# Performance work log

Measured on AMD Instinct MI355X. Metric: run time of the kernel, lower is better.

Reference implementation:

```python
import jax, jax.numpy as jnp
import numpy as np

SL, BS, HS = 2048, 2, 1024
FFN, E, TOP_K = 4096, 8, 2


def setup_inputs() -> dict:
    key = jax.random.key(0)
    k1, k2, k3, k4, k5 = jax.random.split(key, 5)
    x = jax.random.normal(k1, (SL, BS, HS), dtype=jnp.float32)
    expert_weights = jax.random.uniform(k2, (SL * BS, TOP_K), dtype=jnp.float32)
    expert_indices = jax.random.randint(k3, (SL * BS, TOP_K), 0, E, dtype=jnp.int32)
    w1 = jax.random.normal(k4, (E, HS, FFN), dtype=jnp.float32) * 0.02
    w2 = jax.random.normal(k5, (E, FFN, HS), dtype=jnp.float32) * 0.02
    return {"x": x, "expert_weights": expert_weights,
            "expert_indices": expert_indices, "w1": w1, "w2": w2}


def reference(x, expert_weights, expert_indices, w1, w2):
    # Dropless MoE: y[t] = sum_k expert_weights[t,k] * MLP_{expert_indices[t,k]}(x[t])
    # Equivalent to megablocks sort/gather/grouped-GEMM/scatter pipeline, expressed
    # as a fixed loop over the (small) expert axis with masked weighted combine.
    sl, bs, hs = x.shape
    xf = x.reshape(-1, hs)                       # [T, hs]
    ew = expert_weights.reshape(xf.shape[0], -1)  # [T, k]
    ei = expert_indices.reshape(xf.shape[0], -1)  # [T, k]
    out = jnp.zeros_like(xf)
    for e in range(w1.shape[0]):
        h = jnp.dot(jax.nn.gelu(jnp.dot(xf, w1[e])), w2[e])   # [T, hs]
        coef = jnp.sum(jnp.where(ei == e, ew, 0.0), axis=-1)  # [T]
        out = out + coef[:, None] * h
    return out.reshape(sl, bs, hs)
```

## Files before the change

kernel.cpp:

```cpp
#include <hip/hip_runtime.h>
#include <stdint.h>

#define SLEN 2048
#define BSZ  2
#define HSZ  1024
#define FFND 4096
#define NEXP 8
#define TOPK 2
#define NTOK (SLEN*BSZ)
#define NSLOT (NTOK*TOPK)

#define BM 128
#define BN 128
#define BK 32
#define SPLITK 2
#define KS (FFND / SPLITK)

using short8 = __attribute__((ext_vector_type(8))) short;
using f32x4  = __attribute__((ext_vector_type(4))) float;

typedef __attribute__((address_space(1))) const unsigned int gu32;
typedef __attribute__((address_space(3))) unsigned int lu32;

__device__ inline void async_copy16(const void* g, void* l){
  __builtin_amdgcn_global_load_lds((gu32*)g, (lu32*)l, 16, 0, 0);
}

__device__ inline unsigned short f2bf(float f){
  unsigned u = __builtin_bit_cast(unsigned, f);
  u += 0x7FFFu + ((u >> 16) & 1u);
  return (unsigned short)(u >> 16);
}

__device__ inline float gelu_tanh(float x){
  float u = 0.7978845608028654f * (x + 0.044715f * x * x * x);
  return 0.5f * x * (1.0f + tanhf(u));
}


__global__ void k_count(const int* __restrict__ ei, int* __restrict__ counts){
  int i = blockIdx.x * blockDim.x + threadIdx.x;
  if (i < NSLOT) atomicAdd(&counts[ei[i]], 1);
}

__global__ void k_scan(const int* __restrict__ counts, int* __restrict__ offsets,
                       int* __restrict__ fill){
  if (threadIdx.x == 0 && blockIdx.x == 0){
    int acc = 0;
    for (int e = 0; e < NEXP; e++){ offsets[e] = acc; fill[e] = acc; acc += counts[e]; }
  }
}

__global__ void k_assign(const int* __restrict__ ei, const float* __restrict__ ew,
                         int* __restrict__ fill, int* __restrict__ rowT,
                         float* __restrict__ rowC){
  int i = blockIdx.x * blockDim.x + threadIdx.x;
  if (i < NSLOT){
    int e = ei[i];
    int slot = atomicAdd(&fill[e], 1);
    rowT[slot] = i >> 1;
    rowC[slot] = ew[i];
  }
}

__global__ void k_gather(const float* __restrict__ x, const int* __restrict__ rowT,
                         unsigned short* __restrict__ Xg){
  int slot = blockIdx.x;
  int t = rowT[slot];
  int c = threadIdx.x * 4;
  float4 v = *(const float4*)(x + (size_t)t * HSZ + c);
  ushort4 o;
  o.x = f2bf(v.x); o.y = f2bf(v.y); o.z = f2bf(v.z); o.w = f2bf(v.w);
  *(ushort4*)(Xg + (size_t)slot * HSZ + c) = o;
}

__global__ __launch_bounds__(256) void k_transpose2(const float* __restrict__ w1,
                                                    const float* __restrict__ w2,
                                                    unsigned short* __restrict__ Wt1,
                                                    unsigned short* __restrict__ Wt2){
  __shared__ unsigned short tile[64][65];
  const int tid = threadIdx.x;
  int z = blockIdx.y;
  const float* src; unsigned short* dst; int R, C, r0, c0;
  if (z < NEXP){
    src = w1 + (size_t)z * HSZ * FFND; dst = Wt1 + (size_t)z * HSZ * FFND;
    R = HSZ; C = FFND;
    c0 = (blockIdx.x & 63) * 64; r0 = (blockIdx.x >> 6) * 64;
  } else {
    z -= NEXP;
    src = w2 + (size_t)z * FFND * HSZ; dst = Wt2 + (size_t)z * FFND * HSZ;
    R = FFND; C = HSZ;
    c0 = (blockIdx.x & 15) * 64; r0 = (blockIdx.x >> 4) * 64;
  }
  #pragma unroll
  for (int p = 0; p < 4; p++){
    int r  = p * 16 + (tid >> 4);
    int cc = (tid & 15) * 4;
    float4 v = *(const float4*)(src + (size_t)(r0 + r) * C + c0 + cc);
    tile[r][cc]   = f2bf(v.x);
    tile[r][cc+1] = f2bf(v.y);
    tile[r][cc+2] = f2bf(v.z);
    tile[r][cc+3] = f2bf(v.w);
  }
  __syncthreads();
  #pragma unroll
  for (int p = 0; p < 4; p++){
    int c  = p * 16 + (tid >> 4);
    int rr = (tid & 15) * 4;
    ushort4 o;
    o.x = tile[rr][c]; o.y = tile[rr+1][c]; o.z = tile[rr+2][c]; o.w = tile[rr+3][c];
    *(ushort4*)(dst + (size_t)(c0 + c) * R + r0 + rr) = o;
  }
}

__device__ inline void gemm_core(const unsigned short* __restrict__ Ag, int lda, int rows,
                                 const unsigned short* __restrict__ Bg, int ldb, int K,
                                 unsigned short* As, unsigned short* Bs,
                                 f32x4 acc[4][4])
{
  const int tid  = threadIdx.x;
  const int lane = tid & 63;
  const int wid  = tid >> 6;
  const int wm   = (wid & 1) * 64;
  const int wn   = (wid >> 1) * 64;
  const int q    = lane >> 4;
  const int l16  = lane & 15;

  for (int k0 = 0; k0 < K; k0 += BK){
    #pragma unroll
    for (int p = 0; p < 2; p++){
      int c  = (wid * 2 + p) * 64 + lane;
      int r  = c >> 2;
      int kp = (c & 3) * 8;
      int ra = min(r, rows - 1);
      async_copy16(Ag + (size_t)ra * lda + k0 + kp, As + (wid * 2 + p) * 512);
      async_copy16(Bg + (size_t)r  * ldb + k0 + kp, Bs + (wid * 2 + p) * 512);
    }
    __syncthreads();

    short8 af[4], bfr[4];
    #pragma unroll
    for (int i = 0; i < 4; i++)
      af[i] = *(const short8*)(As + (wm + i * 16 + l16) * BK + q * 8);
    #pragma unroll
    for (int j = 0; j < 4; j++)
      bfr[j] = *(const short8*)(Bs + (wn + j * 16 + l16) * BK + q * 8);

    #pragma unroll
    for (int i = 0; i < 4; i++)
      #pragma unroll
      for (int j = 0; j < 4; j++)
        acc[i][j] = __builtin_amdgcn_mfma_f32_16x16x32_bf16(af[i], bfr[j], acc[i][j], 0, 0, 0);
    __syncthreads();
  }
}

__global__ __launch_bounds__(256) void k_gemm1(const unsigned short* __restrict__ Xg,
                                               const unsigned short* __restrict__ Wt1,
                                               unsigned short* __restrict__ H,
                                               const int* __restrict__ counts,
                                               const int* __restrict__ offsets)
{
  __shared__ unsigned short smem[BM * BK + BN * BK];
  unsigned short* As = smem;
  unsigned short* Bs = smem + BM * BK;
  const int e    = blockIdx.z;
  const int cnt  = counts[e];
  const int mblk = blockIdx.y;
  if (mblk * BM >= cnt) return;
  const int n0   = blockIdx.x * BN;
  const int row0 = offsets[e] + mblk * BM;
  const int rows = min(BM, cnt - mblk * BM);

  f32x4 acc[4][4] = {};
  gemm_core(Xg + (size_t)row0 * HSZ, HSZ, rows,
            Wt1 + (size_t)e * HSZ * FFND + (size_t)n0 * HSZ, HSZ, HSZ, As, Bs, acc);

  const int lane = threadIdx.x & 63, wid = threadIdx.x >> 6;
  const int wm = (wid & 1) * 64, wn = (wid >> 1) * 64;
  const int q = lane >> 4, l16 = lane & 15;

  unsigned short* scr = smem + wid * (16 * 68);
  #pragma unroll
  for (int i = 0; i < 4; i++){
    #pragma unroll
    for (int j = 0; j < 4; j++)
      #pragma unroll
      for (int r = 0; r < 4; r++)
        scr[(q * 4 + r) * 68 + j * 16 + l16] = f2bf(gelu_tanh(acc[i][j][r]));
    #pragma unroll
    for (int p = 0; p < 2; p++){
      int rr = p * 8 + (lane >> 3);
      int cc = (lane & 7) * 8;
      short8 v = *(const short8*)(scr + rr * 68 + cc);
      int grow = wm + i * 16 + rr;
      if (grow < rows)
        *(short8*)(H + (size_t)(row0 + grow) * FFND + n0 + wn + cc) = v;
    }
  }
}

__global__ __launch_bounds__(256) void k_gemm2(const unsigned short* __restrict__ H,
                                               const unsigned short* __restrict__ Wt2,
                                               float* __restrict__ out,
                                               const int* __restrict__ counts,
                                               const int* __restrict__ offsets,
                                               const int* __restrict__ rowT,
                                               const float* __restrict__ rowC)
{
  __shared__ unsigned short As[BM * BK];
  __shared__ unsigned short Bs[BN * BK];
  const int e    = blockIdx.z >> 1;
  const int s    = blockIdx.z & 1;
  const int cnt  = counts[e];
  const int mblk = blockIdx.y;
  if (mblk * BM >= cnt) return;
  const int n0   = blockIdx.x * BN;
  const int row0 = offsets[e] + mblk * BM;
  const int rows = min(BM, cnt - mblk * BM);

  f32x4 acc[4][4] = {};
  gemm_core(H + (size_t)row0 * FFND + (size_t)s * KS, FFND, rows,
            Wt2 + (size_t)e * FFND * HSZ + (size_t)n0 * FFND + (size_t)s * KS,
            FFND, KS, As, Bs, acc);

  const int lane = threadIdx.x & 63, wid = threadIdx.x >> 6;
  const int wm = (wid & 1) * 64, wn = (wid >> 1) * 64;
  const int q = lane >> 4, l16 = lane & 15;
  #pragma unroll
  for (int i = 0; i < 4; i++)
    #pragma unroll
    for (int j = 0; j < 4; j++)
      #pragma unroll
      for (int r = 0; r < 4; r++){
        int row = wm + i * 16 + q * 4 + r;
        if (row < rows){
          int g = row0 + row;
          int col = wn + j * 16 + l16;
          atomicAdd(out + (size_t)rowT[g] * HSZ + n0 + col, rowC[g] * acc[i][j][r]);
        }
      }
}

static inline size_t align_up(size_t v, size_t a){ return (v + a - 1) & ~(a - 1); }

extern "C" void kernel_launch(void* const* d_in, const int* in_sizes, int n_in,
                              void* d_out, int out_size, void* d_ws, size_t ws_size,
                              hipStream_t stream) {
  const float* x  = (const float*)d_in[0];
  const float* ew = (const float*)d_in[1];
  const int*   ei = (const int*)d_in[2];
  const float* w1 = (const float*)d_in[3];
  const float* w2 = (const float*)d_in[4];
  float* out = (float*)d_out;

  char* base = (char*)d_ws;
  size_t off = 0;
  int* counts  = (int*)(base + off); off += 64;
  int* fill    = (int*)(base + off); off += 64;
  int* offsets = (int*)(base + off); off = align_up(off + 64, 4096);
  int* rowT    = (int*)(base + off); off += (size_t)NSLOT * 4;
  float* rowC  = (float*)(base + off); off = align_up(off + (size_t)NSLOT * 4, 1 << 20);
  unsigned short* Xg  = (unsigned short*)(base + off); off = align_up(off + (size_t)NSLOT * HSZ * 2, 1 << 20);
  unsigned short* H   = (unsigned short*)(base + off); off = align_up(off + (size_t)NSLOT * FFND * 2, 1 << 20);
  unsigned short* Wt1 = (unsigned short*)(base + off); off = align_up(off + (size_t)NEXP * HSZ * FFND * 2, 1 << 20);
  unsigned short* Wt2 = (unsigned short*)(base + off); off += (size_t)NEXP * FFND * HSZ * 2;
  (void)ws_size;

  hipMemsetAsync(d_out, 0, (size_t)out_size * sizeof(float), stream);
  hipMemsetAsync(counts, 0, 64, stream);

  k_count <<<NSLOT / 256, 256, 0, stream>>>(ei, counts);
  k_scan  <<<1, 64, 0, stream>>>(counts, offsets, fill);
  k_assign<<<NSLOT / 256, 256, 0, stream>>>(ei, ew, fill, rowT, rowC);
  k_gather<<<NSLOT, 256, 0, stream>>>(x, rowT, Xg);

  k_transpose2<<<dim3(1024, 2 * NEXP), 256, 0, stream>>>(w1, w2, Wt1, Wt2);

  k_gemm1<<<dim3(FFND / BN, 64, NEXP), 256, 0, stream>>>(Xg, Wt1, H, counts, offsets);
  k_gemm2<<<dim3(HSZ / BN, 64, NEXP * SPLITK), 256, 0, stream>>>(H, Wt2, out, counts, offsets, rowT, rowC);
}
```

Baseline: 700.6 us.

## Double-buffer GEMM LDS tiles, fuse routing into one kernel, drop split-K

The GEMM core now double-buffers its LDS tiles. It issues the async global-to-LDS loads for the next K-step before computing the current one, which removes one barrier per iteration and overlaps memory with MFMA work. The three routing kernels (count, scan, assign) become a single one-block kernel using shared-memory histograms, which saves launches and a memset. GEMM2 drops split-K, halving the output atomics, but each block now runs the full K loop with half as many blocks and double the LDS per block. The slot order within an expert can differ, but the result is unaffected.

After: 616.7 us. 12.0% less time.

```diff
diff --git a/kernel.cpp b/kernel.cpp
--- a/kernel.cpp
+++ b/kernel.cpp
@@ -13,8 +13,7 @@
 #define BM 128
 #define BN 128
 #define BK 32
-#define SPLITK 2
-#define KS (FFND / SPLITK)
+#define STAGE (BM * BK)
 
 using short8 = __attribute__((ext_vector_type(8))) short;
 using f32x4  = __attribute__((ext_vector_type(4))) float;
@@ -37,27 +36,35 @@
   return 0.5f * x * (1.0f + tanhf(u));
 }
 
-
-__global__ void k_count(const int* __restrict__ ei, int* __restrict__ counts){
-  int i = blockIdx.x * blockDim.x + threadIdx.x;
-  if (i < NSLOT) atomicAdd(&counts[ei[i]], 1);
-}
-
-__global__ void k_scan(const int* __restrict__ counts, int* __restrict__ offsets,
-                       int* __restrict__ fill){
-  if (threadIdx.x == 0 && blockIdx.x == 0){
+__global__ __launch_bounds__(1024) void k_route(const int* __restrict__ ei,
+                                                const float* __restrict__ ew,
+                                                int* __restrict__ counts,
+                                                int* __restrict__ offsets,
+                                                int* __restrict__ rowT,
+                                                float* __restrict__ rowC){
+  __shared__ int hist[NEXP];
+  __shared__ int fill[NEXP];
+  const int tid = threadIdx.x;
+  if (tid < NEXP) hist[tid] = 0;
+  __syncthreads();
+  int myE[NSLOT / 1024];
+  #pragma unroll
+  for (int p = 0; p < NSLOT / 1024; p++){
+    myE[p] = ei[tid + p * 1024];
+    atomicAdd(&hist[myE[p]], 1);
+  }
+  __syncthreads();
+  if (tid == 0){
     int acc = 0;
-    for (int e = 0; e < NEXP; e++){ offsets[e] = acc; fill[e] = acc; acc += counts[e]; }
-  }
-}
-
-__global__ void k_assign(const int* __restrict__ ei, const float* __restrict__ ew,
-                         int* __restrict__ fill, int* __restrict__ rowT,
-                         float* __restrict__ rowC){
-  int i = blockIdx.x * blockDim.x + threadIdx.x;
-  if (i < NSLOT){
-    int e = ei[i];
-    int slot = atomicAdd(&fill[e], 1);
+    for (int e = 0; e < NEXP; e++){
+      offsets[e] = acc; counts[e] = hist[e]; fill[e] = acc; acc += hist[e];
+    }
+  }
+  __syncthreads();
+  #pragma unroll
+  for (int p = 0; p < NSLOT / 1024; p++){
+    int i = tid + p * 1024;
+    int slot = atomicAdd(&fill[myE[p]], 1);
     rowT[slot] = i >> 1;
     rowC[slot] = ew[i];
   }
@@ -126,32 +133,39 @@
   const int q    = lane >> 4;
   const int l16  = lane & 15;
 
-  for (int k0 = 0; k0 < K; k0 += BK){
+  auto stage = [&](int k0, int s){
     #pragma unroll
     for (int p = 0; p < 2; p++){
       int c  = (wid * 2 + p) * 64 + lane;
       int r  = c >> 2;
       int kp = (c & 3) * 8;
       int ra = min(r, rows - 1);
-      async_copy16(Ag + (size_t)ra * lda + k0 + kp, As + (wid * 2 + p) * 512);
-      async_copy16(Bg + (size_t)r  * ldb + k0 + kp, Bs + (wid * 2 + p) * 512);
+      async_copy16(Ag + (size_t)ra * lda + k0 + kp, As + s * STAGE + (wid * 2 + p) * 512);
+      async_copy16(Bg + (size_t)r  * ldb + k0 + kp, Bs + s * STAGE + (wid * 2 + p) * 512);
     }
+  };
+
+  const int niter = K / BK;
+  stage(0, 0);
+  for (int k = 0; k < niter; k++){
     __syncthreads();
+    if (k + 1 < niter) stage((k + 1) * BK, (k + 1) & 1);
+    const unsigned short* Ak = As + (k & 1) * STAGE;
+    const unsigned short* Bk = Bs + (k & 1) * STAGE;
 
     short8 af[4], bfr[4];
     #pragma unroll
     for (int i = 0; i < 4; i++)
-      af[i] = *(const short8*)(As + (wm + i * 16 + l16) * BK + q * 8);
+      af[i] = *(const short8*)(Ak + (wm + i * 16 + l16) * BK + q * 8);
     #pragma unroll
     for (int j = 0; j < 4; j++)
-      bfr[j] = *(const short8*)(Bs + (wn + j * 16 + l16) * BK + q * 8);
+      bfr[j] = *(const short8*)(Bk + (wn + j * 16 + l16) * BK + q * 8);
 
     #pragma unroll
     for (int i = 0; i < 4; i++)
       #pragma unroll
       for (int j = 0; j < 4; j++)
         acc[i][j] = __builtin_amdgcn_mfma_f32_16x16x32_bf16(af[i], bfr[j], acc[i][j], 0, 0, 0);
-    __syncthreads();
   }
 }
 
@@ -161,9 +175,9 @@
                                                const int* __restrict__ counts,
                                                const int* __restrict__ offsets)
 {
-  __shared__ unsigned short smem[BM * BK + BN * BK];
+  __shared__ unsigned short smem[4 * STAGE];
   unsigned short* As = smem;
-  unsigned short* Bs = smem + BM * BK;
+  unsigned short* Bs = smem + 2 * STAGE;
   const int e    = blockIdx.z;
   const int cnt  = counts[e];
   const int mblk = blockIdx.y;
@@ -175,6 +189,7 @@
   f32x4 acc[4][4] = {};
   gemm_core(Xg + (size_t)row0 * HSZ, HSZ, rows,
             Wt1 + (size_t)e * HSZ * FFND + (size_t)n0 * HSZ, HSZ, HSZ, As, Bs, acc);
+  __syncthreads();
 
   const int lane = threadIdx.x & 63, wid = threadIdx.x >> 6;
   const int wm = (wid & 1) * 64, wn = (wid >> 1) * 64;
@@ -208,10 +223,10 @@
                                                const int* __restrict__ rowT,
                                                const float* __restrict__ rowC)
 {
-  __shared__ unsigned short As[BM * BK];
-  __shared__ unsigned short Bs[BN * BK];
-  const int e    = blockIdx.z >> 1;
-  const int s    = blockIdx.z & 1;
+  __shared__ unsigned short smem[4 * STAGE];
+  unsigned short* As = smem;
+  unsigned short* Bs = smem + 2 * STAGE;
+  const int e    = blockIdx.z;
   const int cnt  = counts[e];
   const int mblk = blockIdx.y;
   if (mblk * BM >= cnt) return;
@@ -220,9 +235,8 @@
   const int rows = min(BM, cnt - mblk * BM);
 
   f32x4 acc[4][4] = {};
-  gemm_core(H + (size_t)row0 * FFND + (size_t)s * KS, FFND, rows,
-            Wt2 + (size_t)e * FFND * HSZ + (size_t)n0 * FFND + (size_t)s * KS,
-            FFND, KS, As, Bs, acc);
+  gemm_core(H + (size_t)row0 * FFND, FFND, rows,
+            Wt2 + (size_t)e * FFND * HSZ + (size_t)n0 * FFND, FFND, FFND, As, Bs, acc);
 
   const int lane = threadIdx.x & 63, wid = threadIdx.x >> 6;
   const int wm = (wid & 1) * 64, wn = (wid >> 1) * 64;
@@ -257,7 +271,6 @@
   char* base = (char*)d_ws;
   size_t off = 0;
   int* counts  = (int*)(base + off); off += 64;
-  int* fill    = (int*)(base + off); off += 64;
   int* offsets = (int*)(base + off); off = align_up(off + 64, 4096);
   int* rowT    = (int*)(base + off); off += (size_t)NSLOT * 4;
   float* rowC  = (float*)(base + off); off = align_up(off + (size_t)NSLOT * 4, 1 << 20);
@@ -268,15 +281,12 @@
   (void)ws_size;
 
   hipMemsetAsync(d_out, 0, (size_t)out_size * sizeof(float), stream);
-  hipMemsetAsync(counts, 0, 64, stream);
-
-  k_count <<<NSLOT / 256, 256, 0, stream>>>(ei, counts);
-  k_scan  <<<1, 64, 0, stream>>>(counts, offsets, fill);
-  k_assign<<<NSLOT / 256, 256, 0, stream>>>(ei, ew, fill, rowT, rowC);
+
+  k_route <<<1, 1024, 0, stream>>>(ei, ew, counts, offsets, rowT, rowC);
   k_gather<<<NSLOT, 256, 0, stream>>>(x, rowT, Xg);
 
   k_transpose2<<<dim3(1024, 2 * NEXP), 256, 0, stream>>>(w1, w2, Wt1, Wt2);
 
   k_gemm1<<<dim3(FFND / BN, 64, NEXP), 256, 0, stream>>>(Xg, Wt1, H, counts, offsets);
-  k_gemm2<<<dim3(HSZ / BN, 64, NEXP * SPLITK), 256, 0, stream>>>(H, Wt2, out, counts, offsets, rowT, rowC);
-}
+  k_gemm2<<<dim3(HSZ / BN, 64, NEXP), 256, 0, stream>>>(H, Wt2, out, counts, offsets, rowT, rowC);
+}
```
